# Optimization experiments

Hardware: AMD Instinct MI355X
Metric: run time of the kernel (lower is better)

## Reference

```python
import jax, jax.numpy as jnp
import numpy as np


def _rotate_matrices(angles):
    # angles: (M, 1) -> rot (M, 2, 2), rows [[c, -s], [s, c]]
    c = jnp.cos(angles)
    s = jnp.sin(angles)
    rot = jnp.stack([jnp.concatenate([c, -s], axis=1),
                     jnp.concatenate([s, c], axis=1)], axis=1)
    return rot, jnp.swapaxes(rot, 1, 2)


def _seq_group_permute(x, mapping, perms, final=False):
    # x: (B, S, d), perms: (d//2, 2, 2)
    B, S, d = x.shape
    if not final:
        x = x[:, :, mapping]
    x = x.reshape(B, S, d // 2, 2)
    x = jnp.einsum('ijmk,mkn->ijmn', x, perms).reshape(B, S, d)
    if final:
        x = x[:, :, mapping]
    return x


def _mat_group_permute_inv(m, mapping, perms_inv, transposed):
    # m: (R, d), perms_inv: (d//2, 2, 2)
    R, d = m.shape
    m = m[:, mapping].reshape(R, d // 2, 2)
    sub = 'imk,mkn->imn' if transposed else 'imk,mnk->imn'
    return jnp.einsum(sub, m, perms_inv).reshape(R, d)


def setup_inputs() -> dict:
    key = jax.random.key(0)
    ks = jax.random.split(key, 8)
    B, S, IN, OUT = 4, 2048, 1024, 4096
    inp = jax.random.normal(ks[0], (B, S, IN), dtype=jnp.float32)
    weight = jax.random.normal(ks[1], (OUT, IN), dtype=jnp.float32) * 0.02
    mask = (jax.random.uniform(ks[2], (OUT, IN)) > 0.5).astype(jnp.float32)
    in_scores = jax.random.normal(ks[3], (IN // 2, 1), dtype=jnp.float32)
    out_scores = jax.random.normal(ks[4], (OUT // 2, 1), dtype=jnp.float32)
    in_mapping = jax.random.permutation(ks[5], IN).astype(jnp.int32)
    out_mapping = jax.random.permutation(ks[6], OUT).astype(jnp.int32)
    out_mapping_reverse = jnp.argsort(out_mapping).astype(jnp.int32)
    return {
        'input': inp,
        'weight': weight,
        'mask': mask,
        'in_permutation_scores': in_scores,
        'out_permutation_scores': out_scores,
        'in_mapping': in_mapping,
        'out_mapping': out_mapping,
        'out_mapping_reverse': out_mapping_reverse,
        'temperature': 1,
    }


def reference(input, weight, mask, in_permutation_scores, out_permutation_scores,
              in_mapping, out_mapping, out_mapping_reverse, temperature):
    in_permut, in_permut_inv = _rotate_matrices(in_permutation_scores)
    out_permut, out_permut_inv = _rotate_matrices(out_permutation_scores)
    # permute + rotate activations on the input side
    s_in = _seq_group_permute(input, in_mapping, in_permut)
    # inverse permute/rotate the weight's input dim, then its output dim
    m2 = _mat_group_permute_inv(weight, in_mapping, in_permut_inv, transposed=False)
    m3 = _mat_group_permute_inv(m2.T, out_mapping, out_permut_inv, transposed=True)
    m3 = m3 * mask.T  # (in, out)
    s_inner = jnp.einsum('bsi,io->bso', s_in, m3)
    s_out = _seq_group_permute(s_inner, out_mapping_reverse, out_permut, final=True)
    return s_out
```

## Files before the change

### kernel.cpp

```cpp
#include <hip/hip_runtime.h>
#include <stdint.h>

#define M_DIM 8192
#define K_DIM 1024
#define N_DIM 4096

typedef int int32x4 __attribute__((ext_vector_type(4)));

__device__ __forceinline__ uint32_t pack4(float a, float b, float c, float d, float inv) {
  int q0 = (int)rintf(a * inv), q1 = (int)rintf(b * inv),
      q2 = (int)rintf(c * inv), q3 = (int)rintf(d * inv);
  q0 = q0 > 127 ? 127 : (q0 < -127 ? -127 : q0);
  q1 = q1 > 127 ? 127 : (q1 < -127 ? -127 : q1);
  q2 = q2 > 127 ? 127 : (q2 < -127 ? -127 : q2);
  q3 = q3 > 127 ? 127 : (q3 < -127 ? -127 : q3);
  return (uint32_t)(q0 & 255) | ((uint32_t)(q1 & 255) << 8) |
         ((uint32_t)(q2 & 255) << 16) | ((uint32_t)(q3 & 255) << 24);
}

__global__ __launch_bounds__(256) void quant_a_kernel(
    const float* __restrict__ input,
    int8_t*      __restrict__ a8,
    float*       __restrict__ sA)
{
  const int wave = threadIdx.x >> 6, lane = threadIdx.x & 63;
  const int row  = blockIdx.x * 4 + wave;
  const float* rp = input + (size_t)row * K_DIM;

  float4 v[4];
  float m = 0.f;
#pragma unroll
  for (int j = 0; j < 4; j++) {
    v[j] = ((const float4*)rp)[j * 64 + lane];
    m = fmaxf(m, fmaxf(fmaxf(fabsf(v[j].x), fabsf(v[j].y)),
                       fmaxf(fabsf(v[j].z), fabsf(v[j].w))));
  }
#pragma unroll
  for (int off = 32; off >= 1; off >>= 1) m = fmaxf(m, __shfl_xor(m, off));

  const float inv = (m > 0.f) ? 127.f / m : 0.f;
  uint32_t* op = (uint32_t*)(a8 + (size_t)row * K_DIM);
#pragma unroll
  for (int j = 0; j < 4; j++)
    op[j * 64 + lane] = pack4(v[j].x, v[j].y, v[j].z, v[j].w, inv);
  if (lane == 0) sA[row] = m * (1.f / 127.f);
}

__global__ __launch_bounds__(256) void build_w_kernel(
    const float* __restrict__ weight,
    const float* __restrict__ mask,
    const float* __restrict__ in_scores,
    const float* __restrict__ out_scores,
    const int*   __restrict__ in_mapping,
    const int*   __restrict__ out_mapping,
    int8_t*      __restrict__ w8,
    float*       __restrict__ sW)
{
  __shared__ float w0[K_DIM], w1[K_DIM];
  __shared__ float o0f[K_DIM], o1f[K_DIM];
  __shared__ float red[8];

  const int mo = blockIdx.x;
  const int t  = threadIdx.x;

  const int r0 = out_mapping[2 * mo];
  const int r1 = out_mapping[2 * mo + 1];

  ((float4*)w0)[t] = ((const float4*)(weight + (size_t)r0 * K_DIM))[t];
  ((float4*)w1)[t] = ((const float4*)(weight + (size_t)r1 * K_DIM))[t];

  const float ao = out_scores[mo];
  const float so = sinf(ao), co = cosf(ao);

  __syncthreads();

#pragma unroll
  for (int s = 0; s < 2; s++) {
    const int mi = t + s * 256;
    const float ai = in_scores[mi];
    const float si = sinf(ai), ci = cosf(ai);
    const int ia0 = in_mapping[2 * mi];
    const int ia1 = in_mapping[2 * mi + 1];

    const float w00 = w0[ia0], w01 = w0[ia1];
    const float w10 = w1[ia0], w11 = w1[ia1];

    float a00 =  ci * w00 + si * w01;
    float a01 = -si * w00 + ci * w01;
    float a10 =  ci * w10 + si * w11;
    float a11 = -si * w10 + ci * w11;

    float b00 = co * a00 - so * a10;
    float b10 = co * a01 - so * a11;
    float b01 = so * a00 + co * a10;
    float b11 = so * a01 + co * a11;

    const float2 mk0 = *(const float2*)&mask[(size_t)(2 * mo) * K_DIM + 2 * mi];
    const float2 mk1 = *(const float2*)&mask[(size_t)(2 * mo + 1) * K_DIM + 2 * mi];
    b00 *= mk0.x; b10 *= mk0.y;
    b01 *= mk1.x; b11 *= mk1.y;

    float c00 =  co * b00 + so * b01;
    float c10 =  co * b10 + so * b11;
    float c01 = -so * b00 + co * b01;
    float c11 = -so * b10 + co * b11;

    o0f[ia0] = ci * c00 - si * c10;
    o0f[ia1] = si * c00 + ci * c10;
    o1f[ia0] = ci * c01 - si * c11;
    o1f[ia1] = si * c01 + ci * c11;
  }

  __syncthreads();

  float m0 = 0.f, m1 = 0.f;
#pragma unroll
  for (int e = 0; e < 4; e++) {
    m0 = fmaxf(m0, fabsf(o0f[4 * t + e]));
    m1 = fmaxf(m1, fabsf(o1f[4 * t + e]));
  }
#pragma unroll
  for (int off = 32; off >= 1; off >>= 1) {
    m0 = fmaxf(m0, __shfl_xor(m0, off));
    m1 = fmaxf(m1, __shfl_xor(m1, off));
  }
  if ((t & 63) == 0) { red[(t >> 6) * 2] = m0; red[(t >> 6) * 2 + 1] = m1; }
  __syncthreads();
  m0 = fmaxf(fmaxf(red[0], red[2]), fmaxf(red[4], red[6]));
  m1 = fmaxf(fmaxf(red[1], red[3]), fmaxf(red[5], red[7]));

  const float inv0 = (m0 > 0.f) ? 127.f / m0 : 0.f;
  const float inv1 = (m1 > 0.f) ? 127.f / m1 : 0.f;

  ((uint32_t*)(w8 + (size_t)r0 * K_DIM))[t] =
      pack4(o0f[4 * t], o0f[4 * t + 1], o0f[4 * t + 2], o0f[4 * t + 3], inv0);
  ((uint32_t*)(w8 + (size_t)r1 * K_DIM))[t] =
      pack4(o1f[4 * t], o1f[4 * t + 1], o1f[4 * t + 2], o1f[4 * t + 3], inv1);
  if (t == 0) { sW[r0] = m0 * (1.f / 127.f); sW[r1] = m1 * (1.f / 127.f); }
}

__device__ __forceinline__ void async_load16(const int8_t* g, int8_t* lds_wave_uniform) {
  __builtin_amdgcn_global_load_lds(
      (const __attribute__((address_space(1))) uint32_t*)g,
      (__attribute__((address_space(3))) uint32_t*)lds_wave_uniform,
      16, 0, 0);
}

__global__ __launch_bounds__(256, 2) void gemm_kernel(
    const int8_t* __restrict__ A,
    const int8_t* __restrict__ BT,
    const float*  __restrict__ sA,
    const float*  __restrict__ sW,
    float* __restrict__ C)
{
  __shared__ __align__(16) int8_t As[2][256 * 64];
  __shared__ __align__(16) int8_t Bs[2][128 * 64];

  const int tid  = threadIdx.x;
  const int w    = tid >> 6;
  const int lane = tid & 63;
  const int quad = lane >> 4;
  const int rr   = lane & 15;
  const int wm2  = w >> 1;
  const int wn2  = w & 1;

  const int flat = blockIdx.x;
  const int swz  = ((flat & 7) << 7) | (flat >> 3);
  const int bm   = swz >> 5;
  const int bn   = swz & 31;

  int32x4 acc[8][4] = {};

  const int8_t* gA[4];
  const int8_t* gB[2];
#pragma unroll
  for (int ii = 0; ii < 4; ii++) {
    const int c   = ii * 256 + tid;
    const int row = c >> 2;
    const int g   = (c & 3) ^ ((row >> 1) & 3);
    gA[ii] = A + (size_t)(bm * 256 + row) * K_DIM + g * 16;
  }
#pragma unroll
  for (int ii = 0; ii < 2; ii++) {
    const int c   = ii * 256 + tid;
    const int row = c >> 2;
    const int g   = (c & 3) ^ ((row >> 1) & 3);
    gB[ii] = BT + (size_t)(bn * 128 + row) * K_DIM + g * 16;
  }

#define STAGE(BUF, KT)                                                        \
  do {                                                                        \
    _Pragma("unroll")                                                         \
    for (int ii_ = 0; ii_ < 4; ii_++)                                         \
      async_load16(gA[ii_] + (KT) * 64, &As[BUF][(ii_ * 256 + w * 64) * 16]); \
    _Pragma("unroll")                                                         \
    for (int ii_ = 0; ii_ < 2; ii_++)                                         \
      async_load16(gB[ii_] + (KT) * 64, &Bs[BUF][(ii_ * 256 + w * 64) * 16]); \
  } while (0)

  int offA[8], offB[4];
#pragma unroll
  for (int i = 0; i < 8; i++) {
    const int r = wm2 * 128 + i * 16 + rr;
    offA[i] = r * 64 + (quad ^ ((r >> 1) & 3)) * 16;
  }
#pragma unroll
  for (int j = 0; j < 4; j++) {
    const int r = wn2 * 64 + j * 16 + rr;
    offB[j] = r * 64 + (quad ^ ((r >> 1) & 3)) * 16;
  }

#define TILE(T, MODE)                                                         \
  {                                                                           \
    const int buf_ = (T) & 1;                                                 \
    const int8_t* asb_ = &As[buf_][0];                                        \
    const int8_t* bsb_ = &Bs[buf_][0];                                        \
    int32x4 af[8], bf[4];                                                     \
    _Pragma("unroll") for (int i_ = 0; i_ < 8; i_++)                          \
      af[i_] = *reinterpret_cast<const int32x4*>(asb_ + offA[i_]);            \
    _Pragma("unroll") for (int j_ = 0; j_ < 4; j_++)                          \
      bf[j_] = *reinterpret_cast<const int32x4*>(bsb_ + offB[j_]);            \
    asm volatile("s_waitcnt lgkmcnt(0)" ::: "memory");                        \
    __builtin_amdgcn_sched_barrier(0);                           \
    __builtin_amdgcn_s_barrier();            \
    if (MODE == 0) STAGE(buf_, (T) + 2);                                      \
    __builtin_amdgcn_s_setprio(1);                                            \
    _Pragma("unroll") for (int i_ = 0; i_ < 8; i_++)                          \
      _Pragma("unroll") for (int j_ = 0; j_ < 4; j_++)                        \
        acc[i_][j_] = __builtin_amdgcn_mfma_i32_16x16x64_i8(                  \
            af[i_], bf[j_], acc[i_][j_], 0, 0, 0);                            \
    __builtin_amdgcn_s_setprio(0);                                            \
    if (MODE == 0)      { asm volatile("s_waitcnt vmcnt(6)" ::: "memory"); }  \
    else if (MODE == 1) { asm volatile("s_waitcnt vmcnt(0)" ::: "memory"); }  \
    if (MODE < 2) __builtin_amdgcn_s_barrier();                               \
  }

  STAGE(0, 0);
  STAGE(1, 1);
  asm volatile("s_waitcnt vmcnt(6)" ::: "memory");
  __builtin_amdgcn_s_barrier();

  for (int t = 0; t < 14; ++t) {
    TILE(t, 0);
  }
  TILE(14, 1);
  TILE(15, 2);

#undef TILE
#undef STAGE

  float sw4[4];
#pragma unroll
  for (int j = 0; j < 4; j++)
    sw4[j] = sW[bn * 128 + wn2 * 64 + j * 16 + rr];

#pragma unroll
  for (int i = 0; i < 8; i++) {
    const int row0 = bm * 256 + wm2 * 128 + i * 16 + quad * 4;
#pragma unroll
    for (int rg = 0; rg < 4; rg++) {
      const float sa = sA[row0 + rg];
#pragma unroll
      for (int j = 0; j < 4; j++) {
        const int col = bn * 128 + wn2 * 64 + j * 16 + rr;
        C[(size_t)(row0 + rg) * N_DIM + col] = (float)acc[i][j][rg] * sa * sw4[j];
      }
    }
  }
}

extern "C" void kernel_launch(void* const* d_in, const int* in_sizes, int n_in,
                              void* d_out, int out_size, void* d_ws, size_t ws_size,
                              hipStream_t stream) {
  const float* input      = (const float*)d_in[0];
  const float* weight     = (const float*)d_in[1];
  const float* mask       = (const float*)d_in[2];
  const float* in_scores  = (const float*)d_in[3];
  const float* out_scores = (const float*)d_in[4];
  const int*   in_mapping = (const int*)d_in[5];
  const int*   out_mapping= (const int*)d_in[6];
  float* out = (float*)d_out;

  int8_t* a8 = (int8_t*)d_ws;
  int8_t* w8 = (int8_t*)d_ws + (size_t)M_DIM * K_DIM;
  float*  sA = (float*)((char*)d_ws + 12 * 1024 * 1024);
  float*  sW = (float*)((char*)d_ws + 12 * 1024 * 1024 + 32 * 1024);

  quant_a_kernel<<<2048, 256, 0, stream>>>(input, a8, sA);

  build_w_kernel<<<2048, 256, 0, stream>>>(
      weight, mask, in_scores, out_scores, in_mapping, out_mapping, w8, sW);

  gemm_kernel<<<1024, 256, 0, stream>>>(a8, w8, sA, sW, out);
}
```

Baseline: 227.9 us.

## Double-buffer MFMA register fragments and prefetch next LDS tile during compute

Restructures the int8 GEMM main loop so the LDS-to-register loads for the next k-tile are issued before the MFMAs of the current tile, using two ping-pong register fragment sets. The global-to-LDS staging is moved after the MFMAs and targets tile T+3, with an extra barrier pair per iteration. Output stores become nontemporal. The aim is to hide LDS read latency behind matrix work, at the cost of higher register pressure and a more intricate barrier and buffer-reuse schedule that could race or reduce occupancy.

```diff
diff --git a/kernel.cpp b/kernel.cpp
--- a/kernel.cpp
+++ b/kernel.cpp
@@ -210,29 +210,32 @@
     offB[j] = r * 64 + (quad ^ ((r >> 1) & 3)) * 16;
   }
 
-#define TILE(T, MODE)                                                         \
+#define TILE(T, CA, CB, NA, NB, MODE)                                         \
   {                                                                           \
-    const int buf_ = (T) & 1;                                                 \
-    const int8_t* asb_ = &As[buf_][0];                                        \
-    const int8_t* bsb_ = &Bs[buf_][0];                                        \
-    int32x4 af[8], bf[4];                                                     \
-    _Pragma("unroll") for (int i_ = 0; i_ < 8; i_++)                          \
-      af[i_] = *reinterpret_cast<const int32x4*>(asb_ + offA[i_]);            \
-    _Pragma("unroll") for (int j_ = 0; j_ < 4; j_++)                          \
-      bf[j_] = *reinterpret_cast<const int32x4*>(bsb_ + offB[j_]);            \
-    asm volatile("s_waitcnt lgkmcnt(0)" ::: "memory");                        \
-    __builtin_amdgcn_sched_barrier(0);                           \
-    __builtin_amdgcn_s_barrier();            \
-    if (MODE == 0) STAGE(buf_, (T) + 2);                                      \
     __builtin_amdgcn_s_setprio(1);                                            \
+    if (MODE < 3) {                                                           \
+      const int nb_ = ((T) + 1) & 1;                                          \
+      _Pragma("unroll") for (int i_ = 0; i_ < 8; i_++)                        \
+        NA[i_] = *reinterpret_cast<const int32x4*>(&As[nb_][offA[i_]]);       \
+      _Pragma("unroll") for (int j_ = 0; j_ < 4; j_++)                        \
+        NB[j_] = *reinterpret_cast<const int32x4*>(&Bs[nb_][offB[j_]]);       \
+    }                                                                         \
     _Pragma("unroll") for (int i_ = 0; i_ < 8; i_++)                          \
       _Pragma("unroll") for (int j_ = 0; j_ < 4; j_++)                        \
         acc[i_][j_] = __builtin_amdgcn_mfma_i32_16x16x64_i8(                  \
-            af[i_], bf[j_], acc[i_][j_], 0, 0, 0);                            \
+            CA[i_], CB[j_], acc[i_][j_], 0, 0, 0);                            \
     __builtin_amdgcn_s_setprio(0);                                            \
-    if (MODE == 0)      { asm volatile("s_waitcnt vmcnt(6)" ::: "memory"); }  \
-    else if (MODE == 1) { asm volatile("s_waitcnt vmcnt(0)" ::: "memory"); }  \
-    if (MODE < 2) __builtin_amdgcn_s_barrier();                               \
+    if (MODE < 3) {                                                           \
+      asm volatile("s_waitcnt lgkmcnt(0)" ::: "memory");                      \
+      __builtin_amdgcn_sched_barrier(0);                                      \
+    }                                                                         \
+    if (MODE <= 1) {                                                          \
+      __builtin_amdgcn_s_barrier();  \
+      if (MODE == 0) STAGE(((T) + 3) & 1, (T) + 3);                           \
+      if (MODE == 0) { asm volatile("s_waitcnt vmcnt(6)" ::: "memory"); }     \
+      else           { asm volatile("s_waitcnt vmcnt(0)" ::: "memory"); }     \
+      __builtin_amdgcn_s_barrier();              \
+    }                                                                         \
   }
 
   STAGE(0, 0);
@@ -240,11 +243,28 @@
   asm volatile("s_waitcnt vmcnt(6)" ::: "memory");
   __builtin_amdgcn_s_barrier();
 
-  for (int t = 0; t < 14; ++t) {
-    TILE(t, 0);
-  }
-  TILE(14, 1);
-  TILE(15, 2);
+  int32x4 afA[8], bfA[4], afB[8], bfB[4];
+#pragma unroll
+  for (int i = 0; i < 8; i++)
+    afA[i] = *reinterpret_cast<const int32x4*>(&As[0][offA[i]]);
+#pragma unroll
+  for (int j = 0; j < 4; j++)
+    bfA[j] = *reinterpret_cast<const int32x4*>(&Bs[0][offB[j]]);
+  asm volatile("s_waitcnt lgkmcnt(0)" ::: "memory");
+  __builtin_amdgcn_sched_barrier(0);
+  __builtin_amdgcn_s_barrier();
+  STAGE(0, 2);
+  asm volatile("s_waitcnt vmcnt(6)" ::: "memory");
+  __builtin_amdgcn_s_barrier();
+
+  for (int t = 0; t < 12; t += 2) {
+    TILE(t,     afA, bfA, afB, bfB, 0);
+    TILE(t + 1, afB, bfB, afA, bfA, 0);
+  }
+  TILE(12, afA, bfA, afB, bfB, 0);
+  TILE(13, afB, bfB, afA, bfA, 1);
+  TILE(14, afA, bfA, afB, bfB, 2);
+  TILE(15, afB, bfB, afA, bfA, 3);
 
 #undef TILE
 #undef STAGE
@@ -263,7 +283,8 @@
 #pragma unroll
       for (int j = 0; j < 4; j++) {
         const int col = bn * 128 + wn2 * 64 + j * 16 + rr;
-        C[(size_t)(row0 + rg) * N_DIM + col] = (float)acc[i][j][rg] * sa * sw4[j];
+        __builtin_nontemporal_store((float)acc[i][j][rg] * sa * sw4[j],
+                                    &C[(size_t)(row0 + rg) * N_DIM + col]);
       }
     }
   }
```

New measurement: 238.4 us. +4.6%, slower.
